# Kernel tuning notes

Hardware: AMD Instinct MI355X
Metric: run time of the kernel (lower is better)

The kernel has to match this reference:

```python
import jax, jax.numpy as jnp
import numpy as np

G = 32          # num graphs
NPG = 512       # nodes per graph
EPG = 4096      # edges per graph
DN = 128        # node/edge feat dim
DP = 64         # node identifier dim d_p
DE_ID = 64      # type identifier dim d_e
H = 768         # hidden_dim
IN_DIM = DN + 2 * DP + DE_ID  # 320


def setup_inputs() -> dict:
    key = jax.random.key(0)
    ks = jax.random.split(key, 9)
    N = G * NPG
    E = G * EPG
    x = jax.random.normal(ks[0], (N, DN), jnp.float32)
    edge_attr = jax.random.normal(ks[1], (E, DN), jnp.float32)
    P = jax.random.normal(ks[2], (N, DP), jnp.float32)  # ORF node identifiers
    E_V = jax.random.normal(ks[3], (1, DE_ID), jnp.float32) * 0.1
    E_E = jax.random.normal(ks[4], (1, DE_ID), jnp.float32) * 0.1
    W = jax.random.normal(ks[5], (H, IN_DIM), jnp.float32) / np.sqrt(IN_DIM)
    b = jnp.zeros((H,), jnp.float32)
    graph_token = jax.random.normal(ks[6], (1, H), jnp.float32) * 0.1
    # edges stay within their graph and are sorted by graph id
    base = jnp.repeat(jnp.arange(G, dtype=jnp.int32) * NPG, EPG)  # [E]
    src = base + jax.random.randint(ks[7], (E,), 0, NPG, jnp.int32)
    dst = base + jax.random.randint(ks[8], (E,), 0, NPG, jnp.int32)
    edge_index = jnp.stack([src, dst], axis=0)  # [2, E]
    batch = jnp.repeat(jnp.arange(G, dtype=jnp.int32), NPG)  # [N]
    return {
        "x": x, "edge_attr": edge_attr, "P": P,
        "E_V": E_V, "E_E": E_E, "W": W, "b": b, "graph_token": graph_token,
        "edge_index": edge_index, "batch": batch,
        "num_graphs": G, "max_node_num": NPG, "max_edge_num": EPG,
    }


def reference(x, edge_attr, P, E_V, E_E, W, b, graph_token,
              edge_index, batch, num_graphs, max_node_num, max_edge_num):
    N = x.shape[0]
    E = edge_index.shape[1]
    Hd = W.shape[0]
    d_e = E_V.shape[1]

    # node tokens: [x | P | P | E_V] @ W^T + b
    X_v = jnp.concatenate([x, P, P, jnp.broadcast_to(E_V, (N, d_e))], axis=1)
    X_v_proj = X_v @ W.T + b  # [N, H]

    # edge tokens: [edge_attr | P_u | P_v | E_E] @ W^T + b
    P_u = P[edge_index[0]]
    P_v = P[edge_index[1]]
    X_e = jnp.concatenate([edge_attr, P_u, P_v, jnp.broadcast_to(E_E, (E, d_e))], axis=1)
    X_e_proj = X_e @ W.T + b  # [E, H]

    # ragged -> padded packing (replaces per-graph python loop)
    ones_n = jnp.ones((N,), jnp.int32)
    node_num = jax.ops.segment_sum(ones_n, batch, num_segments=num_graphs)  # [G]
    node_ptr = jnp.cumsum(node_num) - node_num  # exclusive prefix sum
    node_pos = jnp.arange(N, dtype=jnp.int32) - node_ptr[batch]  # position within graph

    edge_batch = batch[edge_index[0]]  # [E]
    ones_e = jnp.ones((E,), jnp.int32)
    edge_num = jax.ops.segment_sum(ones_e, edge_batch, num_segments=num_graphs)
    edge_ptr = jnp.cumsum(edge_num) - edge_num
    edge_pos = jnp.arange(E, dtype=jnp.int32) - edge_ptr[edge_batch]

    seq_len = 1 + max_node_num + max_edge_num  # +1 for [graph] token
    tokens = jnp.zeros((num_graphs, seq_len, Hd), X_v_proj.dtype)
    tokens = tokens.at[:, 0, :].set(graph_token[0])
    tokens = tokens.at[batch, 1 + node_pos].set(X_v_proj)
    tokens = tokens.at[edge_batch, 1 + max_node_num + edge_pos].set(X_e_proj)

    attention_masks = jnp.zeros((num_graphs, seq_len), bool)
    attention_masks = attention_masks.at[:, 0].set(True)
    attention_masks = attention_masks.at[batch, 1 + node_pos].set(True)
    attention_masks = attention_masks.at[edge_batch, 1 + max_node_num + edge_pos].set(True)

    return tokens, attention_masks
```

## Files before the change

kernel.cpp:

```cpp
#include <hip/hip_runtime.h>
#include <stdint.h>

#define NG   32
#define NPG  512
#define EPG  4096
#define DN   128
#define DP   64
#define NN   (NG*NPG)
#define NE   (NG*EPG)
#define KD   320
#define HD   768
#define SEQ  (1+NPG+EPG)
#define TOK_ELEMS ((size_t)NG*SEQ*HD)
#define MASK_ELEMS ((size_t)NG*SEQ)

typedef unsigned short u16;
typedef __attribute__((ext_vector_type(8))) __bf16 bf16x8;
typedef __attribute__((ext_vector_type(8))) short  s16x8;
typedef __attribute__((ext_vector_type(4))) float  f32x4;

__device__ __forceinline__ u16 f2bf(float f) {
    uint32_t u = __builtin_bit_cast(uint32_t, f);
    u += 0x7fffu + ((u >> 16) & 1u);
    return (u16)(u >> 16);
}

__device__ __forceinline__ int b_off(int row, int kb) {
    return ((row >> 1) << 7) + ((row & 1) << 6) + (kb ^ (((row >> 1) & 3) << 4));
}

__global__ void ptr_k(const int* __restrict__ batch, const int* __restrict__ eidx,
                      int* __restrict__ nptr, int* __restrict__ eptr) {
    int t = threadIdx.x;
    if (t < NG) {
        int g = t, lo = 0, hi = NN;
        while (lo < hi) { int mid = (lo + hi) >> 1; if (batch[mid] < g) lo = mid + 1; else hi = mid; }
        nptr[g] = lo;
    } else if (t < 2 * NG) {
        int g = t - NG, lo = 0, hi = NE;
        while (lo < hi) { int mid = (lo + hi) >> 1; if (batch[eidx[mid]] < g) lo = mid + 1; else hi = mid; }
        eptr[g] = lo;
    }
}

__global__ void wconv_k(const float* __restrict__ W, u16* __restrict__ Wb) {
    int i = blockIdx.x * 256 + threadIdx.x;
    if (i < KD * HD) Wb[i] = f2bf(W[i]);
}

__global__ void aux_k(const float* __restrict__ gt, float* __restrict__ out) {
    size_t i = (size_t)blockIdx.x * 256 + threadIdx.x;
    if (i < (size_t)NG * HD) {
        int g = (int)(i / HD), c = (int)(i % HD);
        out[(size_t)g * SEQ * HD + c] = gt[c];
    } else {
        size_t m = i - (size_t)NG * HD;
        if (m < MASK_ELEMS) out[TOK_ELEMS + m] = 1.0f;
    }
}

__global__ __launch_bounds__(256, 2)
void gemm_scatter(const float* __restrict__ x,  const float* __restrict__ ea,
                  const float* __restrict__ P,  const float* __restrict__ EV,
                  const float* __restrict__ EEv,const float* __restrict__ bias,
                  const int* __restrict__ eidx, const int* __restrict__ batch,
                  const u16* __restrict__ Wb,   const int* __restrict__ nptr,
                  const int* __restrict__ eptr, float* __restrict__ out)
{
    __shared__ __align__(16) char b_lds[3][16384];
    __shared__ int info_src[128], info_pu[128], info_pv[128], info_orow[128];

    const int tid  = threadIdx.x;
    const int lane = tid & 63;
    const int wid  = tid >> 6;
    const int lrow = lane & 15;
    const int lq   = lane >> 4;

    uint32_t lconst[4];
    uint32_t ldsoff[4];
    #pragma unroll
    for (int i = 0; i < 4; ++i) {
        uint32_t q   = (uint32_t)((wid * 4 + i) * 1024 + lane * 16);
        uint32_t sub = q >> 13;
        uint32_t qq  = q & 8191u;
        uint32_t row = 2 * (qq >> 7) + ((qq >> 6) & 1);
        uint32_t kb  = (qq & 0x30u) ^ (((qq >> 7) & 3u) << 4);
        lconst[i] = row * (KD * 2) + sub * 64 + kb;
        ldsoff[i] = (uint32_t)((wid * 4 + i) * 1024);
    }
    const char* WbB = (const char*)Wb;

    auto issue_tile = [&](int p) {
        const int nt = p / 5, kp = p - nt * 5;
        const uint32_t base = (uint32_t)(nt * (128 * KD * 2) + kp * 128);
        char* lb = &b_lds[p % 3][0];
        #pragma unroll
        for (int i = 0; i < 4; ++i) {
            __builtin_amdgcn_global_load_lds(
                (const uint32_t*)(WbB + base + lconst[i]),
                (uint32_t*)(lb + ldsoff[i]), 16, 0, 0);
        }
    };

    issue_tile(0);
    issue_tile(1);

    const int r0  = blockIdx.x * 128;
    const bool isNode = (r0 < NN);
    const float* feat = isNode ? x  : ea;
    const float* idv  = isNode ? EV : EEv;

    if (tid < 128) {
        int r = r0 + tid;
        if (isNode) {
            int g = batch[r];
            info_src[tid] = r; info_pu[tid] = r; info_pv[tid] = r;
            info_orow[tid] = g * SEQ + 1 + (r - nptr[g]);
        } else {
            int e = r - NN;
            int s = eidx[e], d = eidx[NE + e];
            int g = batch[s];
            info_src[tid] = e; info_pu[tid] = s; info_pv[tid] = d;
            info_orow[tid] = g * SEQ + 1 + NPG + (e - eptr[g]);
        }
    }
    __syncthreads();

    bf16x8 afr[2][10];
    int obase[2][4];
    #pragma unroll
    for (int rb = 0; rb < 2; ++rb) {
        const int arow = wid * 32 + rb * 16 + lrow;
        const int fsrc = info_src[arow];
        const int pu   = info_pu[arow];
        const int pv   = info_pv[arow];
        #pragma unroll
        for (int s = 0; s < 10; ++s) {
            const int kg = s * 32 + lq * 8;
            const float* sp;
            if      (s < 4) sp = feat + (size_t)fsrc * DN + kg;
            else if (s < 6) sp = P + (size_t)pu * DP + (kg - DN);
            else if (s < 8) sp = P + (size_t)pv * DP + (kg - DN - DP);
            else            sp = idv + (kg - DN - 2 * DP);
            f32x4 f0 = *reinterpret_cast<const f32x4*>(sp);
            f32x4 f1 = *reinterpret_cast<const f32x4*>(sp + 4);
            s16x8 v;
            v[0]=(short)f2bf(f0[0]); v[1]=(short)f2bf(f0[1]);
            v[2]=(short)f2bf(f0[2]); v[3]=(short)f2bf(f0[3]);
            v[4]=(short)f2bf(f1[0]); v[5]=(short)f2bf(f1[1]);
            v[6]=(short)f2bf(f1[2]); v[7]=(short)f2bf(f1[3]);
            afr[rb][s] = __builtin_bit_cast(bf16x8, v);
        }
        #pragma unroll
        for (int j = 0; j < 4; ++j)
            obase[rb][j] = info_orow[wid * 32 + rb * 16 + lq * 4 + j] * HD;
    }

    const int roff = b_off(lrow, lq * 16);

    int pglob = 0;
    for (int nt = 0; nt < 6; ++nt) {
        const int n0 = nt * 128;
        f32x4 acc[2][8];
        #pragma unroll
        for (int rb = 0; rb < 2; ++rb)
            #pragma unroll
            for (int i = 0; i < 8; ++i) acc[rb][i] = (f32x4)0.f;

        #pragma unroll
        for (int kp = 0; kp < 5; ++kp, ++pglob) {
            asm volatile("s_waitcnt vmcnt(4)" ::: "memory");
            __builtin_amdgcn_sched_barrier(0);
            __builtin_amdgcn_s_barrier();
            __builtin_amdgcn_sched_barrier(0);
            {
                int pn = pglob + 2; if (pn > 29) pn = 29;
                issue_tile(pn);
            }
            const char* bb = &b_lds[pglob % 3][0];
            #pragma unroll
            for (int kk = 0; kk < 2; ++kk) {
                const int kt = kp * 2 + kk;
                const char* bs = bb + kk * 8192;
                #pragma unroll
                for (int ni = 0; ni < 8; ++ni) {
                    bf16x8 bf = *reinterpret_cast<const bf16x8*>(bs + ni * 1024 + roff);
                    acc[0][ni] = __builtin_amdgcn_mfma_f32_16x16x32_bf16(afr[0][kt], bf, acc[0][ni], 0, 0, 0);
                    acc[1][ni] = __builtin_amdgcn_mfma_f32_16x16x32_bf16(afr[1][kt], bf, acc[1][ni], 0, 0, 0);
                }
            }
        }

        #pragma unroll
        for (int ni = 0; ni < 8; ++ni) {
            float bv = bias[n0 + ni * 16 + lrow];
            #pragma unroll
            for (int rb = 0; rb < 2; ++rb)
                #pragma unroll
                for (int j = 0; j < 4; ++j)
                    out[obase[rb][j] + n0 + ni * 16 + lrow] = acc[rb][ni][j] + bv;
        }
    }
}

extern "C" void kernel_launch(void* const* d_in, const int* in_sizes, int n_in,
                              void* d_out, int out_size, void* d_ws, size_t ws_size,
                              hipStream_t stream) {
    const float* x    = (const float*)d_in[0];
    const float* ea   = (const float*)d_in[1];
    const float* P    = (const float*)d_in[2];
    const float* EV   = (const float*)d_in[3];
    const float* EEv  = (const float*)d_in[4];
    const float* W    = (const float*)d_in[5];
    const float* bias = (const float*)d_in[6];
    const float* gt   = (const float*)d_in[7];
    const int* eidx   = (const int*)d_in[8];
    const int* batch  = (const int*)d_in[9];

    float* out = (float*)d_out;
    u16* Wb  = (u16*)d_ws;
    int* ints = (int*)((char*)d_ws + (size_t)KD * HD * 2);
    int *nptr = ints, *eptr = ints + 32;

    ptr_k<<<1, 64, 0, stream>>>(batch, eidx, nptr, eptr);
    wconv_k<<<(KD * HD + 255) / 256, 256, 0, stream>>>(W, Wb);
    aux_k<<<(int)(((size_t)NG * HD + MASK_ELEMS + 255) / 256), 256, 0, stream>>>(gt, out);
    gemm_scatter<<<dim3((NN + NE) / 128), 256, 0, stream>>>(
        x, ea, P, EV, EEv, bias, eidx, batch, Wb, nptr, eptr, out);
}
```

Measured before the change: 198.1 us.

## Replace direct global-to-LDS triple buffering with register-staged double buffering

Swaps the async global_load_lds path, which used three LDS stages, for a register prefetch of the next W tile followed by ds_write into a two-stage LDS buffer. Global load addressing is now row-contiguous per thread, and the swizzle moves into the LDS write offsets. This halves one LDS buffer and may give the compiler more freedom to schedule loads. The cost is extra VGPRs for the staged tile, explicit LDS write traffic, and only one stage of prefetch distance to hide global latency.

Measured after the change: 169.3 us. -14.6%, faster.

```diff
diff --git a/kernel.cpp b/kernel.cpp
--- a/kernel.cpp
+++ b/kernel.cpp
@@ -67,7 +67,7 @@
                   const u16* __restrict__ Wb,   const int* __restrict__ nptr,
                   const int* __restrict__ eptr, float* __restrict__ out)
 {
-    __shared__ __align__(16) char b_lds[3][16384];
+    __shared__ __align__(16) char b_lds[2][16384];
     __shared__ int info_src[128], info_pu[128], info_pv[128], info_orow[128];
 
     const int tid  = threadIdx.x;
@@ -76,34 +76,14 @@
     const int lrow = lane & 15;
     const int lq   = lane >> 4;
 
-    uint32_t lconst[4];
-    uint32_t ldsoff[4];
+    uint32_t g_off[4], l_off[4];
     #pragma unroll
     for (int i = 0; i < 4; ++i) {
-        uint32_t q   = (uint32_t)((wid * 4 + i) * 1024 + lane * 16);
-        uint32_t sub = q >> 13;
-        uint32_t qq  = q & 8191u;
-        uint32_t row = 2 * (qq >> 7) + ((qq >> 6) & 1);
-        uint32_t kb  = (qq & 0x30u) ^ (((qq >> 7) & 3u) << 4);
-        lconst[i] = row * (KD * 2) + sub * 64 + kb;
-        ldsoff[i] = (uint32_t)((wid * 4 + i) * 1024);
+        uint32_t u = (uint32_t)(i * 256 + tid);
+        g_off[i] = (u >> 3) * (KD * 2) + (u & 7) * 16;
+        l_off[i] = (((u >> 2) & 1) * 8192u) + (uint32_t)b_off(u >> 3, (u & 3) * 16);
     }
     const char* WbB = (const char*)Wb;
-
-    auto issue_tile = [&](int p) {
-        const int nt = p / 5, kp = p - nt * 5;
-        const uint32_t base = (uint32_t)(nt * (128 * KD * 2) + kp * 128);
-        char* lb = &b_lds[p % 3][0];
-        #pragma unroll
-        for (int i = 0; i < 4; ++i) {
-            __builtin_amdgcn_global_load_lds(
-                (const uint32_t*)(WbB + base + lconst[i]),
-                (uint32_t*)(lb + ldsoff[i]), 16, 0, 0);
-        }
-    };
-
-    issue_tile(0);
-    issue_tile(1);
 
     const int r0  = blockIdx.x * 128;
     const bool isNode = (r0 < NN);
@@ -158,7 +138,13 @@
 
     const int roff = b_off(lrow, lq * 16);
 
-    int pglob = 0;
+    s16x8 pre[4];
+    #pragma unroll
+    for (int i = 0; i < 4; ++i)
+        pre[i] = *reinterpret_cast<const s16x8*>(WbB + g_off[i]);
+
+    int cur = 0;
+    int nxt = 1;
     for (int nt = 0; nt < 6; ++nt) {
         const int n0 = nt * 128;
         f32x4 acc[2][8];
@@ -168,16 +154,23 @@
             for (int i = 0; i < 8; ++i) acc[rb][i] = (f32x4)0.f;
 
         #pragma unroll
-        for (int kp = 0; kp < 5; ++kp, ++pglob) {
-            asm volatile("s_waitcnt vmcnt(4)" ::: "memory");
+        for (int kp = 0; kp < 5; ++kp) {
+            cur ^= 1;
+            char* bb = &b_lds[0][0] + cur * 16384;
+            #pragma unroll
+            for (int i = 0; i < 4; ++i)
+                *reinterpret_cast<s16x8*>(bb + l_off[i]) = pre[i];
+            {
+                int tn  = (nxt < 30) ? nxt : 29; ++nxt;
+                int ntn = tn / 5, kpn = tn - ntn * 5;
+                const char* gb = WbB + (size_t)ntn * (128 * KD * 2) + kpn * 128;
+                #pragma unroll
+                for (int i = 0; i < 4; ++i)
+                    pre[i] = *reinterpret_cast<const s16x8*>(gb + g_off[i]);
+            }
+            asm volatile("s_waitcnt lgkmcnt(0)" ::: "memory");
             __builtin_amdgcn_sched_barrier(0);
             __builtin_amdgcn_s_barrier();
-            __builtin_amdgcn_sched_barrier(0);
-            {
-                int pn = pglob + 2; if (pn > 29) pn = 29;
-                issue_tile(pn);
-            }
-            const char* bb = &b_lds[pglob % 3][0];
             #pragma unroll
             for (int kk = 0; kk < 2; ++kk) {
                 const int kt = kp * 2 + kk;
```
